# Kernel optimization log

Measured on AMD Instinct MI355X. Metric: run time of the kernel, lower is better.

Reference implementation:

```python
import jax, jax.numpy as jnp
import numpy as np

CHANNEL_N = 16
RESET_PROB = 0.5
ALIVE_THRESH = 0.1


def _perceive_kernel(c):
    # Faithful reproduction of the TF kernel construction:
    # stack([sobel_x, sobel_y, identity], axis=0) -> (3,3,3); expand_dims(-2);
    # repeat over channels -> (3,3,C,3). Depthwise conv treats axis0 as filter
    # height and the last axis as the channel multiplier (same as tf code).
    sx = jnp.array([[-1.0, 0.0, 1.0], [-2.0, 0.0, 2.0], [-1.0, 0.0, 1.0]], jnp.float32) / 8.0
    sy = sx.T
    ident = jnp.zeros((3, 3), jnp.float32).at[1, 1].set(1.0)
    k = jnp.stack([sx, sy, ident], axis=0)          # (3,3,3)
    k = jnp.repeat(k[:, :, None, :], c, axis=2)     # (3,3,C,3)
    # TF depthwise output ordering: out_ch = c*multiplier + m -> flatten (C,3)
    return k.reshape(3, 3, 1, c * 3)                # HWIO for grouped conv


def _alive_mask(x):
    # 3x3 max-pool (stride 1, SAME) on alpha channel, thresholded.
    alpha = x[..., 3:4]
    pooled = jax.lax.reduce_window(alpha, -jnp.inf, jax.lax.max,
                                   (1, 3, 3, 1), (1, 1, 1, 1), 'SAME')
    return pooled > ALIVE_THRESH


def setup_inputs() -> dict:
    key = jax.random.key(0)
    k1, k2, k3, k4, k5, k6 = jax.random.split(key, 6)
    B, H, W, C = 32, 256, 256, CHANNEL_N
    x = jax.random.uniform(k1, (B, H, W, C), dtype=jnp.float32)
    rand_mask = jax.random.uniform(k2, (B, H, W, 1), dtype=jnp.float32)
    W1 = jax.random.normal(k3, (3 * C, 128), dtype=jnp.float32) * 0.1
    b1 = jax.random.normal(k4, (128,), dtype=jnp.float32) * 0.1
    W2 = jax.random.normal(k5, (128, C), dtype=jnp.float32) * 0.1
    b2 = jax.random.normal(k6, (C,), dtype=jnp.float32) * 0.1
    return {"x": x, "rand_mask": rand_mask, "W1": W1, "b1": b1, "W2": W2, "b2": b2}


def reference(x, rand_mask, W1, b1, W2, b2):
    C = x.shape[-1]
    pre_update_mask = _alive_mask(x)
    # perceive: depthwise stencil conv, multiplier 3 -> (N,H,W,3C)
    kern = _perceive_kernel(C)
    y = jax.lax.conv_general_dilated(
        x, kern, window_strides=(1, 1), padding='SAME',
        dimension_numbers=('NHWC', 'HWIO', 'NHWC'), feature_group_count=C)
    # rule model: per-cell 1x1 MLP
    h = jax.nn.relu(jnp.einsum('nhwk,kd->nhwd', y, W1) + b1)
    dx = jnp.einsum('nhwd,dc->nhwc', h, W2) + b2
    # stochastic update mask
    upd = (rand_mask < RESET_PROB).astype(x.dtype)
    x = x + dx * upd
    post_update_mask = _alive_mask(x)
    life_mask = jnp.logical_and(pre_update_mask, post_update_mask).astype(x.dtype)
    return x * life_mask
```

## Files before the change

kernel.cpp:

```cpp
#include <hip/hip_runtime.h>

typedef __bf16 bf16x8 __attribute__((ext_vector_type(8)));
typedef float f32x4 __attribute__((ext_vector_type(4)));

#define XS_COLS 130
#define XS_CHP_B 32
#define XS_SLOT_B (XS_COLS * XS_CHP_B)
#define H_BYTES 32768
#define OFF_XS H_BYTES
#define SMEM_BYTES (H_BYTES + 4 * XS_SLOT_B)

__device__ __forceinline__ unsigned short bfbits(float f) {
    __bf16 b = (__bf16)f;
    return __builtin_bit_cast(unsigned short, b);
}

__global__ __launch_bounds__(512, 4) void nca_main(
    const float* __restrict__ x, const float* __restrict__ rm,
    const float* __restrict__ W1, const float* __restrict__ b1,
    const float* __restrict__ W2, const float* __restrict__ b2,
    float* __restrict__ out, unsigned int* __restrict__ am)
{
    __shared__ __align__(16) char smem[SMEM_BYTES];
    char* Hb  = smem;
    char* XSb = smem + OFF_XS;

    const int tid  = threadIdx.x;
    const int lane = tid & 63;
    const int wid  = tid >> 6;
    const int lrow = lane & 15;
    const int kg   = lane >> 4;
    const int kgh  = kg >> 1;
    const int kgl  = kg & 1;

    int raw = blockIdx.x;
    int wg  = (raw & 7) * 256 + (raw >> 3);
    int img = wg >> 6;
    int rem = wg & 63;
    int w0  = (rem >> 5) << 7;
    int h0  = (rem & 31) * 8;

    const size_t imgbase = (size_t)img * 65536;

    const int r  = wid >> 1;
    const int cq = wid & 1;

    bf16x8 wt[2][3];
    #pragma unroll
    for (int m = 0; m < 2; ++m) {
        int n = (r * 2 + m) * 16 + lrow;
        #pragma unroll
        for (int kk = 0; kk < 3; ++kk) {
            float c0, c1, c2;
            if (kk == 0) {
                c0 = kgh ? -0.25f : -0.125f; c1 = 0.f; c2 = kgh ? 0.25f : 0.125f;
            } else if (kk == 1) {
                c0 = kgh ? -0.125f : -0.125f;
                c1 = kgh ? -0.25f  : 0.f;
                c2 = kgh ? -0.125f : 0.125f;
            } else {
                c0 = kgh ? 0.f : 0.125f; c1 = kgh ? 1.f : 0.25f; c2 = kgh ? 0.f : 0.125f;
            }
            bf16x8 v;
            #pragma unroll
            for (int j = 0; j < 8; ++j) {
                int ch = kgl * 8 + j;
                float wv = c0 * W1[(3 * ch + 0) * 128 + n]
                         + c1 * W1[(3 * ch + 1) * 128 + n]
                         + c2 * W1[(3 * ch + 2) * 128 + n];
                v[j] = (__bf16)wv;
            }
            wt[m][kk] = v;
        }
    }

    bf16x8 w2f[4];
    #pragma unroll
    for (int kk = 0; kk < 4; ++kk) {
        bf16x8 v;
        #pragma unroll
        for (int j = 0; j < 8; ++j) {
            int k = kk * 32 + kg * 8 + j;
            v[j] = (__bf16)W2[k * 16 + lrow];
        }
        w2f[kk] = v;
    }

    f32x4 b1q[2];
    #pragma unroll
    for (int m = 0; m < 2; ++m)
        b1q[m] = *reinterpret_cast<const f32x4*>(b1 + (r * 2 + m) * 16 + kg * 4);
    const f32x4 b2q = *reinterpret_cast<const f32x4*>(b2 + kg * 4);

    #pragma unroll
    for (int rr = 0; rr < 3; ++rr) {
        int gh = h0 - 1 + rr;
        int slot = (gh + 4) & 3;
        for (int idx = tid; idx < 520; idx += 512) {
            int col = idx >> 2, chq = idx & 3;
            int gw = w0 + col - 1;
            float4 v = make_float4(0.f, 0.f, 0.f, 0.f);
            if (gh >= 0 && gh < 256 && gw >= 0 && gw < 256)
                v = *reinterpret_cast<const float4*>(x + (imgbase + (size_t)gh * 256 + gw) * 16 + chq * 4);
            ushort4 q = { bfbits(v.x), bfbits(v.y), bfbits(v.z), bfbits(v.w) };
            *reinterpret_cast<ushort4*>(XSb + slot * XS_SLOT_B + col * XS_CHP_B + chq * 8) = q;
        }
    }
    __syncthreads();

    for (int i = 0; i < 8; ++i) {
        int h = h0 + i;
        int sbm = ((h + 3) & 3) * XS_SLOT_B;
        int sb0 = ((h + 4) & 3) * XS_SLOT_B;
        int sbp = ((h + 5) & 3) * XS_SLOT_B;

        #pragma unroll
        for (int t = 0; t < 4; ++t) {
            int pxl = cq * 64 + t * 16 + lrow;
            int colbase = (pxl + 1) * XS_CHP_B + kgl * 16;
            const char* a0p = XSb + sbm + colbase + (kgh ? 0 : -XS_CHP_B);
            const char* a1p = kgh ? (XSb + sb0 + colbase - XS_CHP_B) : (XSb + sbm + colbase + XS_CHP_B);
            const char* a2p = kgh ? (XSb + sbp + colbase)            : (XSb + sb0 + colbase + XS_CHP_B);
            bf16x8 bf0 = *reinterpret_cast<const bf16x8*>(a0p);
            bf16x8 bf1 = *reinterpret_cast<const bf16x8*>(a1p);
            bf16x8 bf2 = *reinterpret_cast<const bf16x8*>(a2p);
            f32x4 a0 = {0.f, 0.f, 0.f, 0.f}, a1 = {0.f, 0.f, 0.f, 0.f};
            a0 = __builtin_amdgcn_mfma_f32_16x16x32_bf16(wt[0][0], bf0, a0, 0, 0, 0);
            a1 = __builtin_amdgcn_mfma_f32_16x16x32_bf16(wt[1][0], bf0, a1, 0, 0, 0);
            a0 = __builtin_amdgcn_mfma_f32_16x16x32_bf16(wt[0][1], bf1, a0, 0, 0, 0);
            a1 = __builtin_amdgcn_mfma_f32_16x16x32_bf16(wt[1][1], bf1, a1, 0, 0, 0);
            a0 = __builtin_amdgcn_mfma_f32_16x16x32_bf16(wt[0][2], bf2, a0, 0, 0, 0);
            a1 = __builtin_amdgcn_mfma_f32_16x16x32_bf16(wt[1][2], bf2, a1, 0, 0, 0);
            #pragma unroll
            for (int m = 0; m < 2; ++m) {
                f32x4 hv = m ? a1 : a0;
                f32x4 bq = b1q[m];
                ushort4 q;
                q.x = bfbits(fmaxf(hv[0] + bq[0], 0.f));
                q.y = bfbits(fmaxf(hv[1] + bq[1], 0.f));
                q.z = bfbits(fmaxf(hv[2] + bq[2], 0.f));
                q.w = bfbits(fmaxf(hv[3] + bq[3], 0.f));
                int n0 = (r * 2 + m) * 16 + kg * 4;
                int chunk = (n0 >> 3) ^ (pxl & 7);
                *reinterpret_cast<ushort4*>(Hb + pxl * 256 + chunk * 16 + ((n0 >> 2) & 1) * 8) = q;
            }
        }
        __syncthreads();

        float4 sv0 = make_float4(0.f, 0.f, 0.f, 0.f), sv1 = make_float4(0.f, 0.f, 0.f, 0.f);
        const bool do_stage = (i < 7);
        const int gh2 = h + 2;
        if (do_stage) {
            int col0 = tid >> 2, chq0 = tid & 3;
            int gw = w0 + col0 - 1;
            if (gh2 < 256 && gw >= 0 && gw < 256)
                sv0 = *reinterpret_cast<const float4*>(x + (imgbase + (size_t)gh2 * 256 + gw) * 16 + chq0 * 4);
            if (tid < 8) {
                int col1 = 128 + (tid >> 2), gw1 = w0 + col1 - 1;
                if (gh2 < 256 && gw1 >= 0 && gw1 < 256)
                    sv1 = *reinterpret_cast<const float4*>(x + (imgbase + (size_t)gh2 * 256 + gw1) * 16 + (tid & 3) * 4);
            }
        }

        const int pxl2 = wid * 16 + lrow;
        f32x4 acc2 = {0.f, 0.f, 0.f, 0.f};
        #pragma unroll
        for (int kk = 0; kk < 4; ++kk) {
            int chunk = (4 * kk + kg) ^ (pxl2 & 7);
            bf16x8 hb = *reinterpret_cast<const bf16x8*>(Hb + pxl2 * 256 + chunk * 16);
            acc2 = __builtin_amdgcn_mfma_f32_16x16x32_bf16(w2f[kk], hb, acc2, 0, 0, 0);
        }

        size_t pix = imgbase + (size_t)h * 256 + w0 + pxl2;
        float upd = (rm[pix] < 0.5f) ? 1.f : 0.f;
        float4 xv = *reinterpret_cast<const float4*>(x + pix * 16 + kg * 4);
        float4 xn;
        xn.x = xv.x + (acc2[0] + b2q[0]) * upd;
        xn.y = xv.y + (acc2[1] + b2q[1]) * upd;
        xn.z = xv.z + (acc2[2] + b2q[2]) * upd;
        xn.w = xv.w + (acc2[3] + b2q[3]) * upd;
        *reinterpret_cast<float4*>(out + pix * 16 + kg * 4) = xn;
        if (kg == 0) {
            unsigned int av = ((unsigned int)bfbits(xv.w) << 16) | (unsigned int)bfbits(xn.w);
            am[pix] = av;
        }

        if (do_stage) {
            int slot = (gh2 + 4) & 3;
            {
                int col0 = tid >> 2, chq0 = tid & 3;
                ushort4 q = { bfbits(sv0.x), bfbits(sv0.y), bfbits(sv0.z), bfbits(sv0.w) };
                *reinterpret_cast<ushort4*>(XSb + slot * XS_SLOT_B + col0 * XS_CHP_B + chq0 * 8) = q;
            }
            if (tid < 8) {
                int col1 = 128 + (tid >> 2);
                ushort4 q = { bfbits(sv1.x), bfbits(sv1.y), bfbits(sv1.z), bfbits(sv1.w) };
                *reinterpret_cast<ushort4*>(XSb + slot * XS_SLOT_B + col1 * XS_CHP_B + (tid & 3) * 8) = q;
            }
        }
        __syncthreads();
    }
}

__global__ __launch_bounds__(256) void nca_life(
    const unsigned int* __restrict__ am, float* __restrict__ out)
{
    int q = blockIdx.x * 256 + threadIdx.x;
    int w = q & 255, hh = (q >> 8) & 255;
    float mn = -1e30f, mo = -1e30f;
    #pragma unroll
    for (int dh = -1; dh <= 1; ++dh) {
        int h2 = hh + dh;
        if (h2 < 0 || h2 > 255) continue;
        #pragma unroll
        for (int dw = -1; dw <= 1; ++dw) {
            int w2 = w + dw;
            if (w2 < 0 || w2 > 255) continue;
            unsigned int v = am[q + dh * 256 + dw];
            mn = fmaxf(mn, __uint_as_float(v << 16));
            mo = fmaxf(mo, __uint_as_float(v & 0xffff0000u));
        }
    }
    if (!(mo > 0.1f && mn > 0.1f)) {
        float4 z = make_float4(0.f, 0.f, 0.f, 0.f);
        float4* o = (float4*)(out + (size_t)q * 16);
        o[0] = z; o[1] = z; o[2] = z; o[3] = z;
    }
}

extern "C" void kernel_launch(void* const* d_in, const int* in_sizes, int n_in,
                              void* d_out, int out_size, void* d_ws, size_t ws_size,
                              hipStream_t stream) {
    (void)in_sizes; (void)n_in; (void)out_size; (void)ws_size;
    const float* x  = (const float*)d_in[0];
    const float* rm = (const float*)d_in[1];
    const float* W1 = (const float*)d_in[2];
    const float* b1 = (const float*)d_in[3];
    const float* W2 = (const float*)d_in[4];
    const float* b2 = (const float*)d_in[5];
    float* out = (float*)d_out;
    unsigned int* am = (unsigned int*)d_ws;

    nca_main<<<dim3(2048), dim3(512), 0, stream>>>(x, rm, W1, b1, W2, b2, out, am);
    nca_life<<<dim3(8192), dim3(256), 0, stream>>>(am, out);
}
```

Baseline: 130.4 us.

## Split row processing into two half-row passes and halve the hidden-activation LDS buffer

Each row is now processed in two 64-pixel halves, so the hidden-activation shared buffer shrinks from 32 KB to 16 KB, which may let more workgroups fit per CU. Warps 0-3 run the second GEMM and epilogue for the first half while warps 4-7 stage the next input row, then the second half runs with warps 4-7 doing its epilogue. This adds two extra barriers per row and halves the per-pass MFMA work per warp, trading synchronisation overhead and idle warps for a smaller LDS footprint and some overlap of staging with compute.

```diff
diff --git a/kernel.cpp b/kernel.cpp
--- a/kernel.cpp
+++ b/kernel.cpp
@@ -6,7 +6,7 @@
 #define XS_COLS 130
 #define XS_CHP_B 32
 #define XS_SLOT_B (XS_COLS * XS_CHP_B)
-#define H_BYTES 32768
+#define H_BYTES 16384
 #define OFF_XS H_BYTES
 #define SMEM_BYTES (H_BYTES + 4 * XS_SLOT_B)
 
@@ -92,32 +92,12 @@
         b1q[m] = *reinterpret_cast<const f32x4*>(b1 + (r * 2 + m) * 16 + kg * 4);
     const f32x4 b2q = *reinterpret_cast<const f32x4*>(b2 + kg * 4);
 
-    #pragma unroll
-    for (int rr = 0; rr < 3; ++rr) {
-        int gh = h0 - 1 + rr;
-        int slot = (gh + 4) & 3;
-        for (int idx = tid; idx < 520; idx += 512) {
-            int col = idx >> 2, chq = idx & 3;
-            int gw = w0 + col - 1;
-            float4 v = make_float4(0.f, 0.f, 0.f, 0.f);
-            if (gh >= 0 && gh < 256 && gw >= 0 && gw < 256)
-                v = *reinterpret_cast<const float4*>(x + (imgbase + (size_t)gh * 256 + gw) * 16 + chq * 4);
-            ushort4 q = { bfbits(v.x), bfbits(v.y), bfbits(v.z), bfbits(v.w) };
-            *reinterpret_cast<ushort4*>(XSb + slot * XS_SLOT_B + col * XS_CHP_B + chq * 8) = q;
-        }
-    }
-    __syncthreads();
-
-    for (int i = 0; i < 8; ++i) {
-        int h = h0 + i;
-        int sbm = ((h + 3) & 3) * XS_SLOT_B;
-        int sb0 = ((h + 4) & 3) * XS_SLOT_B;
-        int sbp = ((h + 5) & 3) * XS_SLOT_B;
-
-        #pragma unroll
-        for (int t = 0; t < 4; ++t) {
-            int pxl = cq * 64 + t * 16 + lrow;
-            int colbase = (pxl + 1) * XS_CHP_B + kgl * 16;
+    auto g1 = [&](int half, int sbm, int sb0, int sbp) {
+        #pragma unroll
+        for (int t = 0; t < 2; ++t) {
+            int pxl = cq * 32 + t * 16 + lrow;
+            int pxg = half * 64 + pxl;
+            int colbase = (pxg + 1) * XS_CHP_B + kgl * 16;
             const char* a0p = XSb + sbm + colbase + (kgh ? 0 : -XS_CHP_B);
             const char* a1p = kgh ? (XSb + sb0 + colbase - XS_CHP_B) : (XSb + sbm + colbase + XS_CHP_B);
             const char* a2p = kgh ? (XSb + sbp + colbase)            : (XSb + sb0 + colbase + XS_CHP_B);
@@ -145,24 +125,10 @@
                 *reinterpret_cast<ushort4*>(Hb + pxl * 256 + chunk * 16 + ((n0 >> 2) & 1) * 8) = q;
             }
         }
-        __syncthreads();
-
-        float4 sv0 = make_float4(0.f, 0.f, 0.f, 0.f), sv1 = make_float4(0.f, 0.f, 0.f, 0.f);
-        const bool do_stage = (i < 7);
-        const int gh2 = h + 2;
-        if (do_stage) {
-            int col0 = tid >> 2, chq0 = tid & 3;
-            int gw = w0 + col0 - 1;
-            if (gh2 < 256 && gw >= 0 && gw < 256)
-                sv0 = *reinterpret_cast<const float4*>(x + (imgbase + (size_t)gh2 * 256 + gw) * 16 + chq0 * 4);
-            if (tid < 8) {
-                int col1 = 128 + (tid >> 2), gw1 = w0 + col1 - 1;
-                if (gh2 < 256 && gw1 >= 0 && gw1 < 256)
-                    sv1 = *reinterpret_cast<const float4*>(x + (imgbase + (size_t)gh2 * 256 + gw1) * 16 + (tid & 3) * 4);
-            }
-        }
-
-        const int pxl2 = wid * 16 + lrow;
+    };
+
+    auto g2epi = [&](int half, int w4, int h) {
+        int pxl2 = w4 * 16 + lrow;
         f32x4 acc2 = {0.f, 0.f, 0.f, 0.f};
         #pragma unroll
         for (int kk = 0; kk < 4; ++kk) {
@@ -170,8 +136,7 @@
             bf16x8 hb = *reinterpret_cast<const bf16x8*>(Hb + pxl2 * 256 + chunk * 16);
             acc2 = __builtin_amdgcn_mfma_f32_16x16x32_bf16(w2f[kk], hb, acc2, 0, 0, 0);
         }
-
-        size_t pix = imgbase + (size_t)h * 256 + w0 + pxl2;
+        size_t pix = imgbase + (size_t)h * 256 + w0 + half * 64 + pxl2;
         float upd = (rm[pix] < 0.5f) ? 1.f : 0.f;
         float4 xv = *reinterpret_cast<const float4*>(x + pix * 16 + kg * 4);
         float4 xn;
@@ -184,20 +149,59 @@
             unsigned int av = ((unsigned int)bfbits(xv.w) << 16) | (unsigned int)bfbits(xn.w);
             am[pix] = av;
         }
-
-        if (do_stage) {
-            int slot = (gh2 + 4) & 3;
-            {
-                int col0 = tid >> 2, chq0 = tid & 3;
-                ushort4 q = { bfbits(sv0.x), bfbits(sv0.y), bfbits(sv0.z), bfbits(sv0.w) };
-                *reinterpret_cast<ushort4*>(XSb + slot * XS_SLOT_B + col0 * XS_CHP_B + chq0 * 8) = q;
-            }
-            if (tid < 8) {
-                int col1 = 128 + (tid >> 2);
-                ushort4 q = { bfbits(sv1.x), bfbits(sv1.y), bfbits(sv1.z), bfbits(sv1.w) };
-                *reinterpret_cast<ushort4*>(XSb + slot * XS_SLOT_B + col1 * XS_CHP_B + (tid & 3) * 8) = q;
-            }
-        }
+    };
+
+    auto stage = [&](int gh2) {
+        int slot = (gh2 + 4) & 3;
+        int tid2 = tid - 256;
+        #pragma unroll
+        for (int k = 0; k < 3; ++k) {
+            int idx = tid2 + k * 256;
+            if (idx < 520) {
+                int col = idx >> 2, chq = idx & 3;
+                int gw = w0 + col - 1;
+                float4 v = make_float4(0.f, 0.f, 0.f, 0.f);
+                if (gh2 < 256 && gw >= 0 && gw < 256)
+                    v = *reinterpret_cast<const float4*>(x + (imgbase + (size_t)gh2 * 256 + gw) * 16 + chq * 4);
+                ushort4 q = { bfbits(v.x), bfbits(v.y), bfbits(v.z), bfbits(v.w) };
+                *reinterpret_cast<ushort4*>(XSb + slot * XS_SLOT_B + col * XS_CHP_B + chq * 8) = q;
+            }
+        }
+    };
+
+    #pragma unroll
+    for (int rr = 0; rr < 3; ++rr) {
+        int gh = h0 - 1 + rr;
+        int slot = (gh + 4) & 3;
+        for (int idx = tid; idx < 520; idx += 512) {
+            int col = idx >> 2, chq = idx & 3;
+            int gw = w0 + col - 1;
+            float4 v = make_float4(0.f, 0.f, 0.f, 0.f);
+            if (gh >= 0 && gh < 256 && gw >= 0 && gw < 256)
+                v = *reinterpret_cast<const float4*>(x + (imgbase + (size_t)gh * 256 + gw) * 16 + chq * 4);
+            ushort4 q = { bfbits(v.x), bfbits(v.y), bfbits(v.z), bfbits(v.w) };
+            *reinterpret_cast<ushort4*>(XSb + slot * XS_SLOT_B + col * XS_CHP_B + chq * 8) = q;
+        }
+    }
+    __syncthreads();
+
+    for (int i = 0; i < 8; ++i) {
+        int h = h0 + i;
+        int sbm = ((h + 3) & 3) * XS_SLOT_B;
+        int sb0 = ((h + 4) & 3) * XS_SLOT_B;
+        int sbp = ((h + 5) & 3) * XS_SLOT_B;
+
+        g1(0, sbm, sb0, sbp);
+        __syncthreads();
+
+        if (wid < 4)      g2epi(0, wid, h);
+        else if (i < 7)   stage(h + 2);
+        __syncthreads();
+
+        g1(1, sbm, sb0, sbp);
+        __syncthreads();
+
+        if (wid >= 4)     g2epi(1, wid - 4, h);
         __syncthreads();
     }
 }
```

After: 138.5 us. +6.2%, slower.
